# Optimization experiments

Measured on AMD Instinct MI355X. Metric: run time of the kernel, lower is better.

Reference implementation:

```python
import jax, jax.numpy as jnp
import numpy as np

EMB = 1024
STEPS = 64
BATCH = 256


def _linear_params(key, fan_in, shape_w, shape_b):
    # torch nn.Linear default init: U(-1/sqrt(fan_in), 1/sqrt(fan_in))
    s = 1.0 / np.sqrt(fan_in)
    k1, k2 = jax.random.split(key)
    W = jax.random.uniform(k1, shape_w, jnp.float32, -s, s)
    b = jax.random.uniform(k2, shape_b, jnp.float32, -s, s)
    return W, b


def setup_inputs() -> dict:
    key = jax.random.key(0)
    ks = jax.random.split(key, 7)
    txt = jax.random.normal(ks[0], (BATCH, STEPS, EMB), jnp.float32)
    W_iu, b_iu = _linear_params(ks[1], EMB, (EMB, EMB), (EMB,))
    W_hu, b_hu = _linear_params(ks[2], EMB, (EMB, EMB), (EMB,))
    W_ir, b_ir = _linear_params(ks[3], EMB, (EMB, EMB), (EMB,))
    W_hr, b_hr = _linear_params(ks[4], EMB, (EMB, EMB), (EMB,))
    W_i, b_i = _linear_params(ks[5], EMB, (EMB, EMB), (EMB,))
    W_h, b_h = _linear_params(ks[6], EMB, (EMB, EMB), (EMB,))
    return {
        "txt": txt,
        "W_iu": W_iu, "b_iu": b_iu, "W_hu": W_hu, "b_hu": b_hu,
        "W_ir": W_ir, "b_ir": b_ir, "W_hr": W_hr, "b_hr": b_hr,
        "W_i": W_i, "b_i": b_i, "W_h": W_h, "b_h": b_h,
    }


def reference(txt, W_iu, b_iu, W_hu, b_hu, W_ir, b_ir, W_hr, b_hr,
              W_i, b_i, W_h, b_h):
    # Step 0: output = tanh(i2h(txt[:, 0]))
    h0 = jnp.tanh(txt[:, 0] @ W_i.T + b_i)  # [B, D]

    # Steps 1..T-1: GRU-style gated update, h carried across time.
    xs = jnp.swapaxes(txt[:, 1:], 0, 1)  # [T-1, B, D]

    def step(h, x):
        update = jax.nn.sigmoid(x @ W_iu.T + b_iu + h @ W_hu.T + b_hu)
        reset = jax.nn.sigmoid(x @ W_ir.T + b_ir + h @ W_hr.T + b_hr)
        cand = jnp.tanh(x @ W_i.T + b_i + (reset * h) @ W_h.T + b_h)
        h_new = update * h + (1.0 - update) * cand
        return h_new, h_new

    _, hs = jax.lax.scan(step, h0, xs)  # hs: [T-1, B, D]
    out = jnp.concatenate([h0[None], hs], axis=0)  # [T, B, D]
    return jnp.swapaxes(out, 0, 1)  # [B, T, D]
```

## Files before the change

kernel.cpp:

```cpp
#include <hip/hip_runtime.h>
#include <hip/hip_bf16.h>
#include <stdint.h>

#define DEV __device__ __forceinline__

typedef __attribute__((ext_vector_type(8))) short short8;
typedef __attribute__((ext_vector_type(4))) float floatx4;

DEV unsigned short f2bf(float f) {
  union { float f; unsigned u; } v; v.f = f;
  return (unsigned short)((v.u + 0x7fffu + ((v.u >> 16) & 1u)) >> 16);
}
DEV float bf2f(unsigned short s) {
  union { unsigned u; float f; } v; v.u = ((unsigned)s) << 16; return v.f;
}
DEV float sigmoid_f(float x) { return 1.0f / (1.0f + __expf(-x)); }
DEV float tanh_f(float x) { return 1.0f - 2.0f / (__expf(2.0f * x) + 1.0f); }

DEV void glds16(const unsigned short* g, unsigned short* l) {
  __builtin_amdgcn_global_load_lds(
      (const __attribute__((address_space(1))) unsigned int*)g,
      (__attribute__((address_space(3))) unsigned int*)l, 16, 0, 0);
}

DEV void store_pair_coh(unsigned* p, unsigned v) {
  __hip_atomic_store(p, v, __ATOMIC_RELAXED, __HIP_MEMORY_SCOPE_AGENT);
}

DEV void groupbar(unsigned* slot) {
  __syncthreads();
  if (threadIdx.x == 0) {
    __hip_atomic_fetch_add(slot, 1u, __ATOMIC_RELAXED, __HIP_MEMORY_SCOPE_AGENT);
    while (__hip_atomic_load(slot, __ATOMIC_RELAXED, __HIP_MEMORY_SCOPE_AGENT) < 32u)
      __builtin_amdgcn_s_sleep(1);
  }
  __syncthreads();
}

#define WAIT_VM(N) asm volatile("s_waitcnt vmcnt(" #N ")" ::: "memory")
#define WAIT_LGKM0 asm volatile("s_waitcnt lgkmcnt(0)" ::: "memory")
#define BAR __builtin_amdgcn_s_barrier()
#define PIN asm volatile("" ::: "memory")

__global__ __launch_bounds__(256, 1) void k_recur(
    const unsigned short* __restrict__ XPur, const unsigned short* __restrict__ Whhc,
    float* __restrict__ out, float* __restrict__ h,
    unsigned short* __restrict__ hbfR, unsigned short* __restrict__ rhbfR,
    const float* __restrict__ b_h, unsigned* __restrict__ bar) {
  __shared__ __align__(16) unsigned short lds[32768];
  const int tid = threadIdx.x;
  const int w = tid >> 6, l = tid & 63;
  const int l15 = l & 15, l4 = l >> 4;
  const int wm = w >> 1, wn = w & 1;
  const int n = blockIdx.x & 31, g = blockIdx.x >> 5;
  const int R0 = g * 32, C0B = n * 32;
  unsigned* slots = bar + g * 128;
  unsigned* hbfRu = (unsigned*)hbfR;
  const unsigned short* WhT = Whhc + (size_t)2048 * 1024;
  const floatx4 z = {0.f, 0.f, 0.f, 0.f};

  short8 BU[32], BR[32];
#pragma unroll
  for (int kg = 0; kg < 32; kg++) {
    BU[kg] = *(const short8*)(Whhc + (size_t)(C0B + wn * 16 + l15) * 1024 + kg * 32 + l4 * 8);
    BR[kg] = *(const short8*)(Whhc + (size_t)(1024 + C0B + wn * 16 + l15) * 1024 + kg * 32 + l4 * 8);
  }

  {
    const int col0 = C0B + (tid & 31);
    const int rb = R0 + (tid >> 5);
#pragma unroll
    for (int r4 = 0; r4 < 4; r4++) {
      const int row = rb + r4 * 8;
      const size_t oidx = (size_t)row * 65536 + col0;
      const float v = tanh_f(out[oidx]);
      out[oidx] = v;
      h[row * 1024 + col0] = v;
      const unsigned mv = (unsigned)f2bf(v);
      const unsigned ov = (unsigned)__shfl_xor((int)mv, 1, 64);
      if ((tid & 1) == 0)
        store_pair_coh(hbfRu + row * 512 + (col0 >> 1), mv | (ov << 16));
    }
  }
  groupbar(slots + 1);

  const int col = C0B + wn * 16 + l15;
  const int erow0 = R0 + wm * 16 + l4 * 4;
  const float bhv = b_h[col];

  float hp[4];
#pragma unroll
  for (int r = 0; r < 4; r++) hp[r] = h[(erow0 + r) * 1024 + col];

  unsigned short xpu[4], xpr[4];
  {
    const unsigned short* XPt = XPur + (size_t)1 * 524288;
#pragma unroll
    for (int r = 0; r < 4; r++) {
      xpu[r] = XPt[(size_t)(erow0 + r) * 2048 + col];
      xpr[r] = XPt[(size_t)(erow0 + r) * 2048 + 1024 + col];
    }
  }

  for (int t = 1; t < 64; t++) {
    const unsigned short* hbfPrev = hbfR + (size_t)(t - 1) * 262144;
    unsigned short* rhbfT = rhbfR + (size_t)(t & 15) * 262144;
    unsigned* rhbfTu = (unsigned*)rhbfT;
    float uu[4], xpi[4];

    {
      PIN;
#pragma unroll
      for (int sc = 0; sc < 4; sc++)
#pragma unroll
        for (int q = 0; q < 4; q++) {
          const int f = q * 4 + w;
          const int kg = sc * 8 + (f >> 1);
          const int rg = f & 1;
          glds16(hbfPrev + (size_t)(R0 + rg * 16 + l15) * 1024 + kg * 32 + l4 * 8,
                 lds + (kg * 2 + rg) * 512);
        }
      floatx4 acc_u = z, acc_r = z;
#define A_SC(sc)                                                               \
  _Pragma("unroll") for (int j = 0; j < 8; j++) {                              \
    const int kg = (sc) * 8 + j;                                               \
    const short8 a = *(const short8*)(lds + (kg * 2 + wm) * 512 + l * 8);      \
    acc_u = __builtin_amdgcn_mfma_f32_16x16x32_bf16(a, BU[kg], acc_u, 0, 0, 0);\
    acc_r = __builtin_amdgcn_mfma_f32_16x16x32_bf16(a, BR[kg], acc_r, 0, 0, 0);\
  }
      WAIT_VM(12); BAR; PIN; A_SC(0)
      WAIT_VM(8);  BAR; PIN; A_SC(1)
      WAIT_VM(4);  BAR; PIN; A_SC(2)
      WAIT_VM(0);  BAR; PIN; A_SC(3)
#undef A_SC
#pragma unroll
      for (int r = 0; r < 4; r++) {
        uu[r] = sigmoid_f(acc_u[r] + bf2f(xpu[r]));
        const float rr = sigmoid_f(acc_r[r] + bf2f(xpr[r]));
        const unsigned mv = (unsigned)f2bf(rr * hp[r]);
        const unsigned ov = (unsigned)__shfl_xor((int)mv, 1, 64);
        if ((l & 1) == 0)
          store_pair_coh(rhbfTu + (erow0 + r) * 512 + (col >> 1), mv | (ov << 16));
      }
    }
#pragma unroll
    for (int r = 0; r < 4; r++)
      xpi[r] = out[((size_t)(erow0 + r) * 64 + t) * 1024 + col];
    groupbar(slots + 2 * t);

    {
      floatx4 acc_c = z;
#define ISSUE_B(h_)                                                            \
  _Pragma("unroll") for (int sc = 0; sc < 4; sc++)                             \
  _Pragma("unroll") for (int q = 0; q < 4; q++) {                              \
    const int f = q * 4 + w;                                                   \
    if (f < 8) {                                                               \
      const int kgl = sc * 4 + (f >> 1), rg = f & 1;                           \
      glds16(rhbfT + (size_t)(R0 + rg * 16 + l15) * 1024 + (h_)*512 + kgl * 32 + l4 * 8, \
             lds + (kgl * 2 + rg) * 512);                                      \
    } else {                                                                   \
      const int kgl = sc * 4 + ((f - 8) >> 1), cg = (f - 8) & 1;               \
      glds16(WhT + (size_t)(C0B + cg * 16 + l15) * 1024 + (h_)*512 + kgl * 32 + l4 * 8, \
             lds + 16384 + (kgl * 2 + cg) * 512);                              \
    }                                                                          \
  }
#define B_SC(sc)                                                               \
  _Pragma("unroll") for (int k = 0; k < 4; k++) {                              \
    const int kgl = (sc) * 4 + k;                                              \
    const short8 a = *(const short8*)(lds + (kgl * 2 + wm) * 512 + l * 8);     \
    const short8 b = *(const short8*)(lds + 16384 + (kgl * 2 + wn) * 512 + l * 8); \
    acc_c = __builtin_amdgcn_mfma_f32_16x16x32_bf16(a, b, acc_c, 0, 0, 0);     \
  }
      PIN;
      ISSUE_B(0)
      WAIT_VM(12); BAR; PIN; B_SC(0)
      WAIT_VM(8);  BAR; PIN; B_SC(1)
      WAIT_VM(4);  BAR; PIN; B_SC(2)
      WAIT_VM(0);  BAR; PIN; B_SC(3)
      WAIT_LGKM0; BAR;
      ISSUE_B(1)
      WAIT_VM(12); BAR; PIN; B_SC(0)
      WAIT_VM(8);  BAR; PIN; B_SC(1)
      WAIT_VM(4);  BAR; PIN; B_SC(2)
      WAIT_VM(0);  BAR; PIN; B_SC(3)
#undef ISSUE_B
#undef B_SC
      unsigned* hbfCu = hbfRu + (size_t)t * 131072;
#pragma unroll
      for (int r = 0; r < 4; r++) {
        const int row = erow0 + r;
        const float cand = tanh_f(acc_c[r] + xpi[r] + bhv);
        const float hn = uu[r] * hp[r] + (1.0f - uu[r]) * cand;
        out[((size_t)row * 64 + t) * 1024 + col] = hn;
        hp[r] = hn;
        const unsigned mv = (unsigned)f2bf(hn);
        const unsigned ov = (unsigned)__shfl_xor((int)mv, 1, 64);
        if ((l & 1) == 0)
          store_pair_coh(hbfCu + row * 512 + (col >> 1), mv | (ov << 16));
      }
    }
    if (t < 63) {
      const unsigned short* XPt = XPur + (size_t)(t + 1) * 524288;
#pragma unroll
      for (int r = 0; r < 4; r++) {
        xpu[r] = XPt[(size_t)(erow0 + r) * 2048 + col];
        xpr[r] = XPt[(size_t)(erow0 + r) * 2048 + 1024 + col];
      }
      groupbar(slots + 2 * t + 1);
    }
  }
}

DEV void gemm128(const unsigned short* __restrict__ A,
                 const unsigned short* __restrict__ B,
                 int tileM, int tileN, floatx4 (&acc)[4][4]) {
  __shared__ __align__(16) unsigned short lds[2][2][4096];
  const int tid = threadIdx.x;
  const int w = tid >> 6, l = tid & 63;
  const int l15 = l & 15, l4 = l >> 4;
  const int wm = w >> 1, wn = w & 1;

  floatx4 z = {0.f, 0.f, 0.f, 0.f};
#pragma unroll
  for (int i = 0; i < 4; i++)
#pragma unroll
    for (int j = 0; j < 4; j++) acc[i][j] = z;

  const unsigned short* ga0 = A + (size_t)(tileM + w * 16 + l15) * 1024 + l4 * 8;
  const unsigned short* ga1 = ga0 + 64 * 1024;
  const unsigned short* gb0 = B + (size_t)(tileN + w * 16 + l15) * 1024 + l4 * 8;
  const unsigned short* gb1 = gb0 + 64 * 1024;

  glds16(ga0, &lds[0][0][w * 512]);
  glds16(ga1, &lds[0][0][(w + 4) * 512]);
  glds16(gb0, &lds[0][1][w * 512]);
  glds16(gb1, &lds[0][1][(w + 4) * 512]);

#pragma unroll 2
  for (int k0 = 0; k0 < 1024; k0 += 32) {
    const int buf = (k0 >> 5) & 1;
    __syncthreads();
    const int kn = k0 + 32;
    if (kn < 1024) {
      const int nb = buf ^ 1;
      glds16(ga0 + kn, &lds[nb][0][w * 512]);
      glds16(ga1 + kn, &lds[nb][0][(w + 4) * 512]);
      glds16(gb0 + kn, &lds[nb][1][w * 512]);
      glds16(gb1 + kn, &lds[nb][1][(w + 4) * 512]);
    }
    short8 af[4], bfr[4];
    const unsigned short* lA = &lds[buf][0][wm * 2048];
    const unsigned short* lB = &lds[buf][1][wn * 2048];
#pragma unroll
    for (int i = 0; i < 4; i++) af[i] = *(const short8*)(lA + i * 512 + l * 8);
#pragma unroll
    for (int j = 0; j < 4; j++) bfr[j] = *(const short8*)(lB + j * 512 + l * 8);
#pragma unroll
    for (int i = 0; i < 4; i++)
#pragma unroll
      for (int j = 0; j < 4; j++)
        acc[i][j] = __builtin_amdgcn_mfma_f32_16x16x32_bf16(af[i], bfr[j], acc[i][j], 0, 0, 0);
  }
}

__global__ __launch_bounds__(256) void k_pre(
    const unsigned short* __restrict__ Xbf, const unsigned short* __restrict__ Wx,
    unsigned short* __restrict__ XPur, float* __restrict__ out,
    const float* __restrict__ b_iu, const float* __restrict__ b_hu,
    const float* __restrict__ b_ir, const float* __restrict__ b_hr,
    const float* __restrict__ b_i) {
  const int tileN = blockIdx.x * 128;
  const int tileM = blockIdx.y * 128;
  floatx4 acc[4][4];
  gemm128(Xbf, Wx, tileM, tileN, acc);
  const int tid = threadIdx.x;
  const int l = tid & 63;
  const int l15 = l & 15, l4 = l >> 4;
  const int wm = (tid >> 6) >> 1, wn = (tid >> 6) & 1;
#pragma unroll
  for (int i = 0; i < 4; i++)
#pragma unroll
    for (int j = 0; j < 4; j++) {
      const int col = tileN + wn * 64 + j * 16 + l15;
      const int rbase = tileM + wm * 64 + i * 16 + l4 * 4;
#pragma unroll
      for (int r = 0; r < 4; r++) {
        const int row = rbase + r;
        const float v = acc[i][j][r];
        if (col < 2048) {
          const float bias = (col < 1024) ? (b_iu[col] + b_hu[col])
                                          : (b_ir[col - 1024] + b_hr[col - 1024]);
          const int b = row >> 6, t = row & 63;
          XPur[(size_t)((t << 8) | b) * 2048 + col] = f2bf(v + bias);
        } else {
          out[(size_t)row * 1024 + (col - 2048)] = v + b_i[col - 2048];
        }
      }
    }
}

__global__ __launch_bounds__(256) void k_conv_txt(const float* __restrict__ x,
                                                  unsigned short* __restrict__ y) {
  const int i = blockIdx.x * 256 + threadIdx.x;
  const float4 v = ((const float4*)x)[i];
  uint2 o;
  o.x = (unsigned)f2bf(v.x) | ((unsigned)f2bf(v.y) << 16);
  o.y = (unsigned)f2bf(v.z) | ((unsigned)f2bf(v.w) << 16);
  ((uint2*)y)[i] = o;
}

__global__ __launch_bounds__(256) void k_conv_w(
    const float* __restrict__ Wiu, const float* __restrict__ Wir, const float* __restrict__ Wi,
    const float* __restrict__ Whu, const float* __restrict__ Whr, const float* __restrict__ Wh,
    unsigned short* __restrict__ Wx, unsigned short* __restrict__ Whh) {
  const int idx = blockIdx.x * 256 + threadIdx.x;
  const int second = idx >= 786432;
  const int id = idx - (second ? 786432 : 0);
  const int n = id >> 8;
  const int kk = (id & 255) << 2;
  const int sel = n >> 10, r = n & 1023;
  const float* src;
  if (second) src = (sel == 0) ? Whu : (sel == 1) ? Whr : Wh;
  else        src = (sel == 0) ? Wiu : (sel == 1) ? Wir : Wi;
  const float4 v = *(const float4*)(src + (size_t)r * 1024 + kk);
  uint2 o;
  o.x = (unsigned)f2bf(v.x) | ((unsigned)f2bf(v.y) << 16);
  o.y = (unsigned)f2bf(v.z) | ((unsigned)f2bf(v.w) << 16);
  unsigned short* dst = second ? Whh : Wx;
  *(uint2*)(dst + (size_t)n * 1024 + kk) = o;
}

extern "C" void kernel_launch(void* const* d_in, const int* in_sizes, int n_in,
                              void* d_out, int out_size, void* d_ws, size_t ws_size,
                              hipStream_t stream) {
  const float* txt  = (const float*)d_in[0];
  const float* Wiu  = (const float*)d_in[1];
  const float* biu  = (const float*)d_in[2];
  const float* Whu  = (const float*)d_in[3];
  const float* bhu  = (const float*)d_in[4];
  const float* Wir  = (const float*)d_in[5];
  const float* bir  = (const float*)d_in[6];
  const float* Whr  = (const float*)d_in[7];
  const float* bhr  = (const float*)d_in[8];
  const float* Wi   = (const float*)d_in[9];
  const float* bi   = (const float*)d_in[10];
  const float* Wh   = (const float*)d_in[11];
  const float* bh   = (const float*)d_in[12];
  float* out = (float*)d_out;

  char* ws = (char*)d_ws;
  unsigned short* Xbf  = (unsigned short*)(ws);
  unsigned short* hbfR = Xbf;
  unsigned short* Wx   = (unsigned short*)(ws + 33554432);
  unsigned short* Whhc = (unsigned short*)(ws + 39845888);
  unsigned short* XPur = (unsigned short*)(ws + 46137344);
  float*          hbuf = (float*)(ws + 113246208);
  unsigned short* rhbfR= (unsigned short*)(ws + 114294784);
  unsigned*       bar  = (unsigned*)(ws + 122683392);

  hipMemsetAsync((void*)bar, 0, 8 * 128 * 4, stream);

  k_conv_txt<<<16384, 256, 0, stream>>>(txt, Xbf);
  k_conv_w<<<6144, 256, 0, stream>>>(Wiu, Wir, Wi, Whu, Whr, Wh, Wx, Whhc);

  k_pre<<<dim3(24, 128), 256, 0, stream>>>(Xbf, Wx, XPur, out, biu, bhu, bir, bhr, bi);

  k_recur<<<256, 256, 0, stream>>>(XPur, Whhc, out, hbuf, hbfR, rhbfR, bh, bar);

  (void)in_sizes; (void)n_in; (void)out_size; (void)ws_size;
}
```

Measured before the change: 1.083 ms.

## Replace counter group barriers with per-block flags polled by a whole wavefront

Replaces the atomic fetch-add counter barrier, where one thread spins with sleep, with per-step, per-block flags. Each block sets its own padded flag, and a wavefront polls all 32 flags of its group in parallel and uses a wave vote to decide when to proceed. The barrier after the hidden-state write is now a poll at the start of the next step, so the wait is deferred to just before the data is needed. This aims to cut barrier latency and atomic contention, at the cost of a larger flag area to memset and busy polling by every wave without sleep.

```diff
diff --git a/kernel.cpp b/kernel.cpp
--- a/kernel.cpp
+++ b/kernel.cpp
@@ -27,14 +27,16 @@
   __hip_atomic_store(p, v, __ATOMIC_RELAXED, __HIP_MEMORY_SCOPE_AGENT);
 }
 
-DEV void groupbar(unsigned* slot) {
-  __syncthreads();
-  if (threadIdx.x == 0) {
-    __hip_atomic_fetch_add(slot, 1u, __ATOMIC_RELAXED, __HIP_MEMORY_SCOPE_AGENT);
-    while (__hip_atomic_load(slot, __ATOMIC_RELAXED, __HIP_MEMORY_SCOPE_AGENT) < 32u)
-      __builtin_amdgcn_s_sleep(1);
-  }
-  __syncthreads();
+DEV void flag_set(unsigned* p) {
+  __hip_atomic_store(p, 1u, __ATOMIC_RELAXED, __HIP_MEMORY_SCOPE_AGENT);
+}
+DEV void poll32(const unsigned* F, int l) {
+  for (;;) {
+    unsigned v = (l < 32)
+        ? __hip_atomic_load(F + (size_t)l * 16, __ATOMIC_RELAXED, __HIP_MEMORY_SCOPE_AGENT)
+        : 1u;
+    if (__all(v != 0)) return;
+  }
 }
 
 #define WAIT_VM(N) asm volatile("s_waitcnt vmcnt(" #N ")" ::: "memory")
@@ -46,7 +48,8 @@
     const unsigned short* __restrict__ XPur, const unsigned short* __restrict__ Whhc,
     float* __restrict__ out, float* __restrict__ h,
     unsigned short* __restrict__ hbfR, unsigned short* __restrict__ rhbfR,
-    const float* __restrict__ b_h, unsigned* __restrict__ bar) {
+    const float* __restrict__ b_h, unsigned* __restrict__ flagR,
+    unsigned* __restrict__ flagH) {
   __shared__ __align__(16) unsigned short lds[32768];
   const int tid = threadIdx.x;
   const int w = tid >> 6, l = tid & 63;
@@ -54,7 +57,6 @@
   const int wm = w >> 1, wn = w & 1;
   const int n = blockIdx.x & 31, g = blockIdx.x >> 5;
   const int R0 = g * 32, C0B = n * 32;
-  unsigned* slots = bar + g * 128;
   unsigned* hbfRu = (unsigned*)hbfR;
   const unsigned short* WhT = Whhc + (size_t)2048 * 1024;
   const floatx4 z = {0.f, 0.f, 0.f, 0.f};
@@ -82,7 +84,8 @@
         store_pair_coh(hbfRu + row * 512 + (col0 >> 1), mv | (ov << 16));
     }
   }
-  groupbar(slots + 1);
+  __syncthreads();
+  if (tid == 0) flag_set(flagH + (size_t)(0 * 8 + g) * 512 + n * 16);
 
   const int col = C0B + wn * 16 + l15;
   const int erow0 = R0 + wm * 16 + l4 * 4;
@@ -108,6 +111,7 @@
     unsigned* rhbfTu = (unsigned*)rhbfT;
     float uu[4], xpi[4];
 
+    poll32(flagH + (size_t)((t - 1) * 8 + g) * 512, l);
     {
       PIN;
 #pragma unroll
@@ -146,8 +150,10 @@
 #pragma unroll
     for (int r = 0; r < 4; r++)
       xpi[r] = out[((size_t)(erow0 + r) * 64 + t) * 1024 + col];
-    groupbar(slots + 2 * t);
-
+    __syncthreads();
+    if (tid == 0) flag_set(flagR + (size_t)(t * 8 + g) * 512 + n * 16);
+
+    poll32(flagR + (size_t)(t * 8 + g) * 512, l);
     {
       floatx4 acc_c = z;
 #define ISSUE_B(h_)                                                            \
@@ -206,7 +212,8 @@
         xpu[r] = XPt[(size_t)(erow0 + r) * 2048 + col];
         xpr[r] = XPt[(size_t)(erow0 + r) * 2048 + 1024 + col];
       }
-      groupbar(slots + 2 * t + 1);
+      __syncthreads();
+      if (tid == 0) flag_set(flagH + (size_t)(t * 8 + g) * 512 + n * 16);
     }
   }
 }
@@ -356,16 +363,18 @@
   unsigned short* XPur = (unsigned short*)(ws + 46137344);
   float*          hbuf = (float*)(ws + 113246208);
   unsigned short* rhbfR= (unsigned short*)(ws + 114294784);
-  unsigned*       bar  = (unsigned*)(ws + 122683392);
-
-  hipMemsetAsync((void*)bar, 0, 8 * 128 * 4, stream);
+  unsigned*       flagR= (unsigned*)(ws + 122683392);
+  unsigned*       flagH= flagR + 262144;
+
+  hipMemsetAsync((void*)flagR, 0, 2097152, stream);
 
   k_conv_txt<<<16384, 256, 0, stream>>>(txt, Xbf);
   k_conv_w<<<6144, 256, 0, stream>>>(Wiu, Wir, Wi, Whu, Whr, Wh, Wx, Whhc);
 
   k_pre<<<dim3(24, 128), 256, 0, stream>>>(Xbf, Wx, XPur, out, biu, bhu, bir, bhr, bi);
 
-  k_recur<<<256, 256, 0, stream>>>(XPur, Whhc, out, hbuf, hbfR, rhbfR, bh, bar);
+  k_recur<<<256, 256, 0, stream>>>(XPur, Whhc, out, hbuf, hbfR, rhbfR, bh,
+                                   flagR, flagH);
 
   (void)in_sizes; (void)n_in; (void)out_size; (void)ws_size;
 }
```

Result: slower. 1.132 ms (+4.5%).
